# Optimization experiments

Hardware: AMD Instinct MI355X
Metric: run time of the kernel (lower is better)

## Reference

```python
import jax, jax.numpy as jnp
import numpy as np

TOP_K = 2


def setup_inputs() -> dict:
    key = jax.random.key(0)
    ks = jax.random.split(key, 5)
    B, S, H, E, I = 2, 1024, 1024, 16, 1024
    scale = 1.0 / np.sqrt(H)
    return {
        "hidden_states": jax.random.normal(ks[0], (B, S, H), dtype=jnp.float32),
        "router_w": jax.random.normal(ks[1], (E, H), dtype=jnp.float32) * scale,   # nn.Linear(H,E).weight
        "gate_w": jax.random.normal(ks[2], (E, I, H), dtype=jnp.float32) * scale,  # per-expert Linear(H,I).weight
        "up_w": jax.random.normal(ks[3], (E, I, H), dtype=jnp.float32) * scale,
        "down_w": jax.random.normal(ks[4], (E, H, I), dtype=jnp.float32) * (1.0 / np.sqrt(I)),
    }


def reference(hidden_states, router_w, gate_w, up_w, down_w):
    orig_shape = hidden_states.shape
    x = hidden_states.reshape(-1, orig_shape[-1])  # [T, H]
    T = x.shape[0]
    E = router_w.shape[0]

    # Router: sigmoid -> top-k -> normalize
    logits = jnp.einsum("th,eh->te", x, router_w)           # [T, E]
    scores = jax.nn.sigmoid(logits)
    weights, indices = jax.lax.top_k(scores, TOP_K)         # [T, K]
    weights = weights / (weights.sum(axis=-1, keepdims=True) + 1e-20)

    # Dense per-token-per-expert combine weight (0 for unrouted pairs) ==
    # exact math of the torch gather/index_add loop.
    w_full = jnp.zeros((T, E), dtype=x.dtype).at[
        jnp.arange(T)[:, None], indices
    ].add(weights)                                          # [T, E]

    # Expert MLPs (SwiGLU) computed for all experts, zero-weighted combine.
    g = jax.nn.silu(jnp.einsum("th,eih->tei", x, gate_w))   # [T, E, I]
    u = jnp.einsum("th,eih->tei", x, up_w)                  # [T, E, I]
    out = jnp.einsum("te,tei,ehi->th", w_full, g * u, down_w)  # [T, H]
    return out.reshape(orig_shape)
```

## Files before the change

kernel.cpp:

```cpp
#include <hip/hip_runtime.h>
#include <stdint.h>

#define T_TOK 2048
#define H_DIM 1024
#define E_NUM 16
#define I_DIM 1024
#define TOTAL_ROWS (2 * T_TOK)
#define CPAD 16

typedef short bf16x8 __attribute__((ext_vector_type(8)));
typedef float f32x4 __attribute__((ext_vector_type(4)));

__device__ __forceinline__ void async_copy16(const void* g, void* l) {
  __builtin_amdgcn_global_load_lds(
      (const __attribute__((address_space(1))) void*)g,
      (__attribute__((address_space(3))) void*)l, 16, 0, 0);
}

__device__ __forceinline__ uint32_t f2bf(float f) {
  uint32_t u = __float_as_uint(f);
  return (u + 0x7FFFu + ((u >> 16) & 1u)) >> 16;
}
__device__ __forceinline__ uint32_t pk2bf(float lo, float hi) {
  return f2bf(lo) | (f2bf(hi) << 16);
}

__global__ __launch_bounds__(256) void router_kernel(
    const float* __restrict__ x, const float* __restrict__ rw,
    uint16_t* __restrict__ xbf, int* __restrict__ counts,
    int* __restrict__ tokens, float* __restrict__ wts) {
  const int t = blockIdx.x * 4 + (threadIdx.x >> 6);
  const int lane = threadIdx.x & 63;

  float4 xv[4];
  float acc[E_NUM];
#pragma unroll
  for (int e = 0; e < E_NUM; ++e) acc[e] = 0.f;

#pragma unroll
  for (int rep = 0; rep < 4; ++rep) {
    const int h0 = rep * 256 + lane * 4;
    xv[rep] = *(const float4*)(x + (size_t)t * H_DIM + h0);
    uint2 p;
    p.x = pk2bf(xv[rep].x, xv[rep].y);
    p.y = pk2bf(xv[rep].z, xv[rep].w);
    *(uint2*)(xbf + (size_t)t * H_DIM + h0) = p;
  }

#pragma unroll
  for (int e = 0; e < E_NUM; ++e) {
#pragma unroll
    for (int rep = 0; rep < 4; ++rep) {
      const float4 rv = *(const float4*)(rw + (size_t)e * H_DIM + rep * 256 + lane * 4);
      acc[e] += xv[rep].x * rv.x + xv[rep].y * rv.y + xv[rep].z * rv.z +
                xv[rep].w * rv.w;
    }
  }

#pragma unroll
  for (int e = 0; e < E_NUM; ++e) {
    float v = acc[e];
#pragma unroll
    for (int off = 32; off > 0; off >>= 1) v += __shfl_xor(v, off);
    acc[e] = v;
  }

  if (lane < 2) {
    float s[E_NUM];
#pragma unroll
    for (int e = 0; e < E_NUM; ++e) s[e] = 1.f / (1.f + expf(-acc[e]));
    int i1 = 0;
    float v1 = s[0];
#pragma unroll
    for (int e = 1; e < E_NUM; ++e)
      if (s[e] > v1) { v1 = s[e]; i1 = e; }
    int i2 = -1;
    float v2 = -1.f;
#pragma unroll
    for (int e = 0; e < E_NUM; ++e)
      if (e != i1 && s[e] > v2) { v2 = s[e]; i2 = e; }
    const float inv = 1.f / (v1 + v2 + 1e-20f);
    const int pe = (lane == 0) ? i1 : i2;
    const float pw = ((lane == 0) ? v1 : v2) * inv;
    const int slot = atomicAdd(&counts[pe * CPAD], 1);
    tokens[pe * T_TOK + slot] = t;
    wts[pe * T_TOK + slot] = pw;
  }
}

__global__ void offsets_kernel(const int* __restrict__ counts,
                               int* __restrict__ offsets) {
  if (threadIdx.x == 0) {
    int a = 0;
    for (int e = 0; e < E_NUM; ++e) {
      offsets[e] = a;
      a += counts[e * CPAD];
    }
    offsets[E_NUM] = a;
  }
}


__global__ __launch_bounds__(512, 4) void gemm1_kernel(
    const uint16_t* __restrict__ xbf, const float* __restrict__ gate,
    const float* __restrict__ up, const int* __restrict__ counts,
    const int* __restrict__ offsets, const int* __restrict__ tokens,
    const float* __restrict__ wts, uint16_t* __restrict__ hbuf) {
  const int e = blockIdx.z;
  const int count = counts[e * CPAD];
  const int m0 = blockIdx.y * 256;
  if (m0 >= count) return;
  const int n0 = blockIdx.x * 64;

  __shared__ __align__(16) uint16_t As[256 * 64];
  __shared__ __align__(16) uint16_t Bgs[64 * 64];
  __shared__ __align__(16) uint16_t Bus[64 * 64];
  __shared__ int tok_s[256];
  __shared__ float wt_s[256];

  const int tid = threadIdx.x;
  if (tid < 256) {
    const int slot = m0 + tid;
    int tk = 0;
    float w = 0.f;
    if (slot < count) {
      tk = tokens[e * T_TOK + slot];
      w = wts[e * T_TOK + slot];
    }
    tok_s[tid] = tk;
    wt_s[tid] = w;
  }
  __syncthreads();

  const uint16_t* a_g[4];
  uint16_t* a_l[4];
#pragma unroll
  for (int j = 0; j < 4; ++j) {
    const int c = j * 512 + tid;
    const int m = c >> 3;
    const int kq = (c & 7) ^ (m & 7);
    a_g[j] = xbf + (size_t)tok_s[m] * H_DIM + kq * 8;
    a_l[j] = As + c * 8;
  }
  const int bm = tid >> 3;
  const int bkq = (tid & 7) ^ (bm & 7);
  const float* g_g = gate + ((size_t)e * I_DIM + n0 + bm) * H_DIM + bkq * 8;
  const float* u_g = up + ((size_t)e * I_DIM + n0 + bm) * H_DIM + bkq * 8;
  uint16_t* bg_l = Bgs + tid * 8;
  uint16_t* bu_l = Bus + tid * 8;

  const int wave = tid >> 6, lane = tid & 63;
  const int wm = (wave & 3) * 64, wn = (wave >> 2) * 32;
  const int lc = lane & 15, lq = lane >> 4;
  const int l7 = lc & 7;

  f32x4 accg[4][2], accu[4][2];
  const f32x4 zero4 = {0.f, 0.f, 0.f, 0.f};
#pragma unroll
  for (int i = 0; i < 4; ++i)
#pragma unroll
    for (int j = 0; j < 2; ++j) {
      accg[i][j] = zero4;
      accu[i][j] = zero4;
    }

  int am[4], bn[2];
#pragma unroll
  for (int i = 0; i < 4; ++i) am[i] = (wm + i * 16 + lc) * 64;
#pragma unroll
  for (int i = 0; i < 2; ++i) bn[i] = (wn + i * 16 + lc) * 64;

  float4 gr0 = *(const float4*)g_g;
  float4 gr1 = *(const float4*)(g_g + 4);
  float4 ur0 = *(const float4*)u_g;
  float4 ur1 = *(const float4*)(u_g + 4);

  for (int k0 = 0; k0 < H_DIM; k0 += 64) {
    __syncthreads();
#pragma unroll
    for (int j = 0; j < 4; ++j) async_copy16(a_g[j] + k0, a_l[j]);
    uint4 p;
    p.x = pk2bf(gr0.x, gr0.y);
    p.y = pk2bf(gr0.z, gr0.w);
    p.z = pk2bf(gr1.x, gr1.y);
    p.w = pk2bf(gr1.z, gr1.w);
    *(uint4*)bg_l = p;
    p.x = pk2bf(ur0.x, ur0.y);
    p.y = pk2bf(ur0.z, ur0.w);
    p.z = pk2bf(ur1.x, ur1.y);
    p.w = pk2bf(ur1.z, ur1.w);
    *(uint4*)bu_l = p;
    __syncthreads();
    if (k0 + 64 < H_DIM) {
      gr0 = *(const float4*)(g_g + k0 + 64);
      gr1 = *(const float4*)(g_g + k0 + 68);
      ur0 = *(const float4*)(u_g + k0 + 64);
      ur1 = *(const float4*)(u_g + k0 + 68);
    }

#pragma unroll
    for (int ks = 0; ks < 2; ++ks) {
      const int kswz = ((ks * 4 + lq) ^ l7) * 8;
      bf16x8 af[4], bg[2], bu[2];
#pragma unroll
      for (int i = 0; i < 4; ++i) af[i] = *(const bf16x8*)(As + am[i] + kswz);
#pragma unroll
      for (int i = 0; i < 2; ++i) {
        bg[i] = *(const bf16x8*)(Bgs + bn[i] + kswz);
        bu[i] = *(const bf16x8*)(Bus + bn[i] + kswz);
      }
#pragma unroll
      for (int im = 0; im < 4; ++im)
#pragma unroll
        for (int in = 0; in < 2; ++in) {
          accg[im][in] = __builtin_amdgcn_mfma_f32_16x16x32_bf16(
              af[im], bg[in], accg[im][in], 0, 0, 0);
          accu[im][in] = __builtin_amdgcn_mfma_f32_16x16x32_bf16(
              af[im], bu[in], accu[im][in], 0, 0, 0);
        }
    }
  }

  const int off_e = offsets[e];
#pragma unroll
  for (int im = 0; im < 4; ++im) {
#pragma unroll
    for (int r = 0; r < 4; ++r) {
      const int row = wm + im * 16 + lq * 4 + r;
      const int slot = m0 + row;
      if (slot < count) {
        const float w = wt_s[row];
        uint16_t* hrow = hbuf + (size_t)(off_e + slot) * I_DIM + n0 + wn;
#pragma unroll
        for (int in = 0; in < 2; ++in) {
          const float g = accg[im][in][r];
          const float u = accu[im][in][r];
          const float hv = g / (1.f + __expf(-g)) * u * w;
          hrow[in * 16 + lc] = (uint16_t)f2bf(hv);
        }
      }
    }
  }
}

__global__ __launch_bounds__(512, 4) void gemm2_kernel(
    const uint16_t* __restrict__ hbuf, const float* __restrict__ down,
    const int* __restrict__ counts, const int* __restrict__ offsets,
    const int* __restrict__ tokens, float* __restrict__ out) {
  const int e = blockIdx.z;
  const int count = counts[e * CPAD];
  const int m0 = blockIdx.y * 256;
  if (m0 >= count) return;
  const int n0 = blockIdx.x * 64;

  __shared__ __align__(16) uint16_t As[256 * 64];
  __shared__ __align__(16) uint16_t Bs[64 * 64];
  __shared__ int tok_s[256];

  const int tid = threadIdx.x;
  const int off_e = offsets[e];
  if (tid < 256) {
    const int slot = m0 + tid;
    tok_s[tid] = (slot < count) ? tokens[e * T_TOK + slot] : 0;
  }

  const uint16_t* a_g[4];
  uint16_t* a_l[4];
#pragma unroll
  for (int j = 0; j < 4; ++j) {
    const int c = j * 512 + tid;
    const int m = c >> 3;
    const int kq = (c & 7) ^ (m & 7);
    int r = off_e + m0 + m;
    if (r > TOTAL_ROWS - 1) r = TOTAL_ROWS - 1;
    a_g[j] = hbuf + (size_t)r * I_DIM + kq * 8;
    a_l[j] = As + c * 8;
  }
  const int bm = tid >> 3;
  const int bkq = (tid & 7) ^ (bm & 7);
  const float* d_g = down + ((size_t)e * H_DIM + n0 + bm) * I_DIM + bkq * 8;
  uint16_t* b_l = Bs + tid * 8;

  const int wave = tid >> 6, lane = tid & 63;
  const int wm = (wave & 3) * 64, wn = (wave >> 2) * 32;
  const int lc = lane & 15, lq = lane >> 4;
  const int l7 = lc & 7;

  f32x4 acc[4][2];
  const f32x4 zero4 = {0.f, 0.f, 0.f, 0.f};
#pragma unroll
  for (int i = 0; i < 4; ++i)
#pragma unroll
    for (int j = 0; j < 2; ++j) acc[i][j] = zero4;

  int am[4], bn[2];
#pragma unroll
  for (int i = 0; i < 4; ++i) am[i] = (wm + i * 16 + lc) * 64;
#pragma unroll
  for (int i = 0; i < 2; ++i) bn[i] = (wn + i * 16 + lc) * 64;

  __syncthreads();

  float4 dr0 = *(const float4*)d_g;
  float4 dr1 = *(const float4*)(d_g + 4);

  for (int k0 = 0; k0 < I_DIM; k0 += 64) {
    __syncthreads();
#pragma unroll
    for (int j = 0; j < 4; ++j) async_copy16(a_g[j] + k0, a_l[j]);
    uint4 p;
    p.x = pk2bf(dr0.x, dr0.y);
    p.y = pk2bf(dr0.z, dr0.w);
    p.z = pk2bf(dr1.x, dr1.y);
    p.w = pk2bf(dr1.z, dr1.w);
    *(uint4*)b_l = p;
    __syncthreads();
    if (k0 + 64 < I_DIM) {
      dr0 = *(const float4*)(d_g + k0 + 64);
      dr1 = *(const float4*)(d_g + k0 + 68);
    }

#pragma unroll
    for (int ks = 0; ks < 2; ++ks) {
      const int kswz = ((ks * 4 + lq) ^ l7) * 8;
      bf16x8 af[4], bf[2];
#pragma unroll
      for (int i = 0; i < 4; ++i) af[i] = *(const bf16x8*)(As + am[i] + kswz);
#pragma unroll
      for (int i = 0; i < 2; ++i) bf[i] = *(const bf16x8*)(Bs + bn[i] + kswz);
#pragma unroll
      for (int im = 0; im < 4; ++im)
#pragma unroll
        for (int in = 0; in < 2; ++in)
          acc[im][in] = __builtin_amdgcn_mfma_f32_16x16x32_bf16(
              af[im], bf[in], acc[im][in], 0, 0, 0);
    }
  }

#pragma unroll
  for (int im = 0; im < 4; ++im) {
#pragma unroll
    for (int r = 0; r < 4; ++r) {
      const int row = wm + im * 16 + lq * 4 + r;
      const int slot = m0 + row;
      if (slot < count) {
        float* orow = out + (size_t)tok_s[row] * H_DIM + n0 + wn;
#pragma unroll
        for (int in = 0; in < 2; ++in)
          atomicAdd(orow + in * 16 + lc, acc[im][in][r]);
      }
    }
  }
}

extern "C" void kernel_launch(void* const* d_in, const int* in_sizes, int n_in,
                              void* d_out, int out_size, void* d_ws,
                              size_t ws_size, hipStream_t stream) {
  const float* x = (const float*)d_in[0];
  const float* rw = (const float*)d_in[1];
  const float* gate = (const float*)d_in[2];
  const float* up = (const float*)d_in[3];
  const float* down = (const float*)d_in[4];
  float* out = (float*)d_out;

  uint8_t* ws = (uint8_t*)d_ws;
  int* counts = (int*)ws;
  int* offsets = (int*)(ws + 2048);
  int* tokens = (int*)(ws + 4096);
  float* wts = (float*)(ws + 4096 + 131072);
  uint16_t* xbf = (uint16_t*)(ws + 4096 + 262144);
  uint16_t* hbuf = (uint16_t*)(ws + 4096 + 262144 + 4194304);

  hipMemsetAsync(counts, 0, 2048, stream);
  hipMemsetAsync(out, 0, (size_t)out_size * sizeof(float), stream);

  router_kernel<<<512, 256, 0, stream>>>(x, rw, xbf, counts, tokens, wts);
  offsets_kernel<<<1, 64, 0, stream>>>(counts, offsets);
  gemm1_kernel<<<dim3(16, 8, 16), 512, 0, stream>>>(
      xbf, gate, up, counts, offsets, tokens, wts, hbuf);
  gemm2_kernel<<<dim3(16, 8, 16), 512, 0, stream>>>(hbuf, down, counts,
                                                    offsets, tokens, out);
}
```

Baseline: 285.0 us.

## Double-buffer LDS tiles and shrink MoE GEMM blocks to 128 rows

Both expert GEMM kernels now double-buffer the A and B shared-memory tiles, so the async load of the next K-slice is issued while MFMAs run on the current one, and one barrier per iteration is removed. The M-tile drops from 256 to 128 rows with 256 threads per block and the grid doubles in y, which cuts padding waste for experts with uneven token counts. Weight tiles are now loaded by two passes per thread. Halving the M-tile means each weight tile is converted and loaded from fp32 twice as often across the grid, which raises weight traffic.

```diff
diff --git a/kernel.cpp b/kernel.cpp
--- a/kernel.cpp
+++ b/kernel.cpp
@@ -101,25 +101,25 @@
 }
 
 
-__global__ __launch_bounds__(512, 4) void gemm1_kernel(
+__global__ __launch_bounds__(256, 2) void gemm1_kernel(
     const uint16_t* __restrict__ xbf, const float* __restrict__ gate,
     const float* __restrict__ up, const int* __restrict__ counts,
     const int* __restrict__ offsets, const int* __restrict__ tokens,
     const float* __restrict__ wts, uint16_t* __restrict__ hbuf) {
   const int e = blockIdx.z;
   const int count = counts[e * CPAD];
-  const int m0 = blockIdx.y * 256;
+  const int m0 = blockIdx.y * 128;
   if (m0 >= count) return;
   const int n0 = blockIdx.x * 64;
 
-  __shared__ __align__(16) uint16_t As[256 * 64];
-  __shared__ __align__(16) uint16_t Bgs[64 * 64];
-  __shared__ __align__(16) uint16_t Bus[64 * 64];
-  __shared__ int tok_s[256];
-  __shared__ float wt_s[256];
+  __shared__ __align__(16) uint16_t As[2][128 * 64];
+  __shared__ __align__(16) uint16_t Bgs[2][64 * 64];
+  __shared__ __align__(16) uint16_t Bus[2][64 * 64];
+  __shared__ int tok_s[128];
+  __shared__ float wt_s[128];
 
   const int tid = threadIdx.x;
-  if (tid < 256) {
+  if (tid < 128) {
     const int slot = m0 + tid;
     int tk = 0;
     float w = 0.f;
@@ -133,24 +133,30 @@
   __syncthreads();
 
   const uint16_t* a_g[4];
-  uint16_t* a_l[4];
+  uint32_t a_lo[4];
 #pragma unroll
   for (int j = 0; j < 4; ++j) {
-    const int c = j * 512 + tid;
+    const int c = j * 256 + tid;
     const int m = c >> 3;
     const int kq = (c & 7) ^ (m & 7);
     a_g[j] = xbf + (size_t)tok_s[m] * H_DIM + kq * 8;
-    a_l[j] = As + c * 8;
-  }
-  const int bm = tid >> 3;
-  const int bkq = (tid & 7) ^ (bm & 7);
-  const float* g_g = gate + ((size_t)e * I_DIM + n0 + bm) * H_DIM + bkq * 8;
-  const float* u_g = up + ((size_t)e * I_DIM + n0 + bm) * H_DIM + bkq * 8;
-  uint16_t* bg_l = Bgs + tid * 8;
-  uint16_t* bu_l = Bus + tid * 8;
+    a_lo[j] = c * 8;
+  }
+  const float* g_g[2];
+  const float* u_g[2];
+  uint32_t b_lo[2];
+#pragma unroll
+  for (int j = 0; j < 2; ++j) {
+    const int c = j * 256 + tid;
+    const int bm = c >> 3;
+    const int kq = (c & 7) ^ (bm & 7);
+    g_g[j] = gate + ((size_t)e * I_DIM + n0 + bm) * H_DIM + kq * 8;
+    u_g[j] = up + ((size_t)e * I_DIM + n0 + bm) * H_DIM + kq * 8;
+    b_lo[j] = c * 8;
+  }
 
   const int wave = tid >> 6, lane = tid & 63;
-  const int wm = (wave & 3) * 64, wn = (wave >> 2) * 32;
+  const int wm = (wave & 1) * 64, wn = (wave >> 1) * 32;
   const int lc = lane & 15, lq = lane >> 4;
   const int l7 = lc & 7;
 
@@ -170,32 +176,45 @@
 #pragma unroll
   for (int i = 0; i < 2; ++i) bn[i] = (wn + i * 16 + lc) * 64;
 
-  float4 gr0 = *(const float4*)g_g;
-  float4 gr1 = *(const float4*)(g_g + 4);
-  float4 ur0 = *(const float4*)u_g;
-  float4 ur1 = *(const float4*)(u_g + 4);
+  float4 gr[2][2], ur[2][2];
+#pragma unroll
+  for (int j = 0; j < 2; ++j) {
+    gr[j][0] = *(const float4*)g_g[j];
+    gr[j][1] = *(const float4*)(g_g[j] + 4);
+    ur[j][0] = *(const float4*)u_g[j];
+    ur[j][1] = *(const float4*)(u_g[j] + 4);
+  }
+#pragma unroll
+  for (int j = 0; j < 4; ++j) async_copy16(a_g[j], &As[0][a_lo[j]]);
 
   for (int k0 = 0; k0 < H_DIM; k0 += 64) {
-    __syncthreads();
-#pragma unroll
-    for (int j = 0; j < 4; ++j) async_copy16(a_g[j] + k0, a_l[j]);
-    uint4 p;
-    p.x = pk2bf(gr0.x, gr0.y);
-    p.y = pk2bf(gr0.z, gr0.w);
-    p.z = pk2bf(gr1.x, gr1.y);
-    p.w = pk2bf(gr1.z, gr1.w);
-    *(uint4*)bg_l = p;
-    p.x = pk2bf(ur0.x, ur0.y);
-    p.y = pk2bf(ur0.z, ur0.w);
-    p.z = pk2bf(ur1.x, ur1.y);
-    p.w = pk2bf(ur1.z, ur1.w);
-    *(uint4*)bu_l = p;
+    const int buf = (k0 >> 6) & 1;
+#pragma unroll
+    for (int j = 0; j < 2; ++j) {
+      uint4 p;
+      p.x = pk2bf(gr[j][0].x, gr[j][0].y);
+      p.y = pk2bf(gr[j][0].z, gr[j][0].w);
+      p.z = pk2bf(gr[j][1].x, gr[j][1].y);
+      p.w = pk2bf(gr[j][1].z, gr[j][1].w);
+      *(uint4*)&Bgs[buf][b_lo[j]] = p;
+      p.x = pk2bf(ur[j][0].x, ur[j][0].y);
+      p.y = pk2bf(ur[j][0].z, ur[j][0].w);
+      p.z = pk2bf(ur[j][1].x, ur[j][1].y);
+      p.w = pk2bf(ur[j][1].z, ur[j][1].w);
+      *(uint4*)&Bus[buf][b_lo[j]] = p;
+    }
     __syncthreads();
     if (k0 + 64 < H_DIM) {
-      gr0 = *(const float4*)(g_g + k0 + 64);
-      gr1 = *(const float4*)(g_g + k0 + 68);
-      ur0 = *(const float4*)(u_g + k0 + 64);
-      ur1 = *(const float4*)(u_g + k0 + 68);
+#pragma unroll
+      for (int j = 0; j < 2; ++j) {
+        gr[j][0] = *(const float4*)(g_g[j] + k0 + 64);
+        gr[j][1] = *(const float4*)(g_g[j] + k0 + 68);
+        ur[j][0] = *(const float4*)(u_g[j] + k0 + 64);
+        ur[j][1] = *(const float4*)(u_g[j] + k0 + 68);
+      }
+#pragma unroll
+      for (int j = 0; j < 4; ++j)
+        async_copy16(a_g[j] + k0 + 64, &As[buf ^ 1][a_lo[j]]);
     }
 
 #pragma unroll
@@ -203,11 +222,12 @@
       const int kswz = ((ks * 4 + lq) ^ l7) * 8;
       bf16x8 af[4], bg[2], bu[2];
 #pragma unroll
-      for (int i = 0; i < 4; ++i) af[i] = *(const bf16x8*)(As + am[i] + kswz);
+      for (int i = 0; i < 4; ++i)
+        af[i] = *(const bf16x8*)&As[buf][am[i] + kswz];
 #pragma unroll
       for (int i = 0; i < 2; ++i) {
-        bg[i] = *(const bf16x8*)(Bgs + bn[i] + kswz);
-        bu[i] = *(const bf16x8*)(Bus + bn[i] + kswz);
+        bg[i] = *(const bf16x8*)&Bgs[buf][bn[i] + kswz];
+        bu[i] = *(const bf16x8*)&Bus[buf][bn[i] + kswz];
       }
 #pragma unroll
       for (int im = 0; im < 4; ++im)
@@ -243,46 +263,53 @@
   }
 }
 
-__global__ __launch_bounds__(512, 4) void gemm2_kernel(
+__global__ __launch_bounds__(256, 2) void gemm2_kernel(
     const uint16_t* __restrict__ hbuf, const float* __restrict__ down,
     const int* __restrict__ counts, const int* __restrict__ offsets,
     const int* __restrict__ tokens, float* __restrict__ out) {
   const int e = blockIdx.z;
   const int count = counts[e * CPAD];
-  const int m0 = blockIdx.y * 256;
+  const int m0 = blockIdx.y * 128;
   if (m0 >= count) return;
   const int n0 = blockIdx.x * 64;
 
-  __shared__ __align__(16) uint16_t As[256 * 64];
-  __shared__ __align__(16) uint16_t Bs[64 * 64];
-  __shared__ int tok_s[256];
+  __shared__ __align__(16) uint16_t As[2][128 * 64];
+  __shared__ __align__(16) uint16_t Bs[2][64 * 64];
+  __shared__ int tok_s[128];
 
   const int tid = threadIdx.x;
   const int off_e = offsets[e];
-  if (tid < 256) {
+  if (tid < 128) {
     const int slot = m0 + tid;
     tok_s[tid] = (slot < count) ? tokens[e * T_TOK + slot] : 0;
   }
+  __syncthreads();
 
   const uint16_t* a_g[4];
-  uint16_t* a_l[4];
+  uint32_t a_lo[4];
 #pragma unroll
   for (int j = 0; j < 4; ++j) {
-    const int c = j * 512 + tid;
+    const int c = j * 256 + tid;
     const int m = c >> 3;
     const int kq = (c & 7) ^ (m & 7);
     int r = off_e + m0 + m;
     if (r > TOTAL_ROWS - 1) r = TOTAL_ROWS - 1;
     a_g[j] = hbuf + (size_t)r * I_DIM + kq * 8;
-    a_l[j] = As + c * 8;
-  }
-  const int bm = tid >> 3;
-  const int bkq = (tid & 7) ^ (bm & 7);
-  const float* d_g = down + ((size_t)e * H_DIM + n0 + bm) * I_DIM + bkq * 8;
-  uint16_t* b_l = Bs + tid * 8;
+    a_lo[j] = c * 8;
+  }
+  const float* d_g[2];
+  uint32_t b_lo[2];
+#pragma unroll
+  for (int j = 0; j < 2; ++j) {
+    const int c = j * 256 + tid;
+    const int bm = c >> 3;
+    const int kq = (c & 7) ^ (bm & 7);
+    d_g[j] = down + ((size_t)e * H_DIM + n0 + bm) * I_DIM + kq * 8;
+    b_lo[j] = c * 8;
+  }
 
   const int wave = tid >> 6, lane = tid & 63;
-  const int wm = (wave & 3) * 64, wn = (wave >> 2) * 32;
+  const int wm = (wave & 1) * 64, wn = (wave >> 1) * 32;
   const int lc = lane & 15, lq = lane >> 4;
   const int l7 = lc & 7;
 
@@ -299,25 +326,36 @@
 #pragma unroll
   for (int i = 0; i < 2; ++i) bn[i] = (wn + i * 16 + lc) * 64;
 
-  __syncthreads();
-
-  float4 dr0 = *(const float4*)d_g;
-  float4 dr1 = *(const float4*)(d_g + 4);
+  float4 dr[2][2];
+#pragma unroll
+  for (int j = 0; j < 2; ++j) {
+    dr[j][0] = *(const float4*)d_g[j];
+    dr[j][1] = *(const float4*)(d_g[j] + 4);
+  }
+#pragma unroll
+  for (int j = 0; j < 4; ++j) async_copy16(a_g[j], &As[0][a_lo[j]]);
 
   for (int k0 = 0; k0 < I_DIM; k0 += 64) {
-    __syncthreads();
-#pragma unroll
-    for (int j = 0; j < 4; ++j) async_copy16(a_g[j] + k0, a_l[j]);
-    uint4 p;
-    p.x = pk2bf(dr0.x, dr0.y);
-    p.y = pk2bf(dr0.z, dr0.w);
-    p.z = pk2bf(dr1.x, dr1.y);
-    p.w = pk2bf(dr1.z, dr1.w);
-    *(uint4*)b_l = p;
+    const int buf = (k0 >> 6) & 1;
+#pragma unroll
+    for (int j = 0; j < 2; ++j) {
+      uint4 p;
+      p.x = pk2bf(dr[j][0].x, dr[j][0].y);
+      p.y = pk2bf(dr[j][0].z, dr[j][0].w);
+      p.z = pk2bf(dr[j][1].x, dr[j][1].y);
+      p.w = pk2bf(dr[j][1].z, dr[j][1].w);
+      *(uint4*)&Bs[buf][b_lo[j]] = p;
+    }
     __syncthreads();
     if (k0 + 64 < I_DIM) {
-      dr0 = *(const float4*)(d_g + k0 + 64);
-      dr1 = *(const float4*)(d_g + k0 + 68);
+#pragma unroll
+      for (int j = 0; j < 2; ++j) {
+        dr[j][0] = *(const float4*)(d_g[j] + k0 + 64);
+        dr[j][1] = *(const float4*)(d_g[j] + k0 + 68);
+      }
+#pragma unroll
+      for (int j = 0; j < 4; ++j)
+        async_copy16(a_g[j] + k0 + 64, &As[buf ^ 1][a_lo[j]]);
     }
 
 #pragma unroll
@@ -325,9 +363,11 @@
       const int kswz = ((ks * 4 + lq) ^ l7) * 8;
       bf16x8 af[4], bf[2];
 #pragma unroll
-      for (int i = 0; i < 4; ++i) af[i] = *(const bf16x8*)(As + am[i] + kswz);
-#pragma unroll
-      for (int i = 0; i < 2; ++i) bf[i] = *(const bf16x8*)(Bs + bn[i] + kswz);
+      for (int i = 0; i < 4; ++i)
+        af[i] = *(const bf16x8*)&As[buf][am[i] + kswz];
+#pragma unroll
+      for (int i = 0; i < 2; ++i)
+        bf[i] = *(const bf16x8*)&Bs[buf][bn[i] + kswz];
 #pragma unroll
       for (int im = 0; im < 4; ++im)
 #pragma unroll
@@ -376,8 +416,8 @@
 
   router_kernel<<<512, 256, 0, stream>>>(x, rw, xbf, counts, tokens, wts);
   offsets_kernel<<<1, 64, 0, stream>>>(counts, offsets);
-  gemm1_kernel<<<dim3(16, 8, 16), 512, 0, stream>>>(
+  gemm1_kernel<<<dim3(16, 16, 16), 256, 0, stream>>>(
       xbf, gate, up, counts, offsets, tokens, wts, hbuf);
-  gemm2_kernel<<<dim3(16, 8, 16), 512, 0, stream>>>(hbuf, down, counts,
-                                                    offsets, tokens, out);
-}
+  gemm2_kernel<<<dim3(16, 16, 16), 256, 0, stream>>>(hbuf, down, counts,
+                                                     offsets, tokens, out);
+}
```

After: 295.6 us. 1.04x slower.
